# Kernel tuning notes

Measured on AMD Instinct MI355X. Metric: run time of the kernel, lower is better.

## Reference

```python
import jax, jax.numpy as jnp
import numpy as np

B, L, C, H = 2, 2048, 1024, 16
D = C // H
THETA = 50000.0


def rotate_half(x):
    x1, x2 = jnp.split(x, 2, axis=-1)
    return jnp.concatenate((-x2, x1), axis=-1)


def rope_freqs(n, dim):
    inv_freq = 1.0 / (THETA ** (jnp.arange(0, dim, 2, dtype=jnp.float32) / dim))
    freqs = jnp.arange(n, dtype=jnp.float32)[:, None] * inv_freq[None, :]  # [n, dim//2]
    return jnp.concatenate((freqs, freqs), axis=-1)  # [n, dim]


def setup_inputs() -> dict:
    key = jax.random.key(0)
    ks = jax.random.split(key, 8)
    q = jax.random.normal(ks[0], (B, L, C), dtype=jnp.float32)
    mask = jax.random.randint(ks[1], (B, L), 0, 2) > 0
    mask = mask.at[:, 0].set(True)  # avoid fully-masked rows
    s = 1.0 / np.sqrt(C)
    Wq = jax.random.normal(ks[2], (C, C), dtype=jnp.float32) * s
    Wk = jax.random.normal(ks[3], (C, C), dtype=jnp.float32) * s
    Wv = jax.random.normal(ks[4], (C, C), dtype=jnp.float32) * s
    Wo = jax.random.normal(ks[5], (C, C), dtype=jnp.float32) * s
    bo = jnp.zeros((C,), dtype=jnp.float32)
    return {"q": q, "mask": mask, "Wq": Wq, "Wk": Wk, "Wv": Wv, "Wo": Wo, "bo": bo}


def reference(q, mask, Wq, Wk, Wv, Wo, bo):
    x = q
    # QKV projections (torch Linear: y = x @ W.T)
    def proj(W):
        y = jnp.einsum('blc,oc->blo', x, W)
        return y.reshape(B, L, H, D).transpose(0, 2, 1, 3)  # [B,H,L,D]
    qh, kh, vh = proj(Wq), proj(Wk), proj(Wv)
    # RoPE (L == S)
    pos = rope_freqs(L, D)  # [L, D]
    cos, sin = jnp.cos(pos), jnp.sin(pos)
    qh = qh * cos + rotate_half(qh) * sin
    kh = kh * cos + rotate_half(kh) * sin
    # masked SDPA with additive bias (-inf where mask is False)
    scale = 1.0 / np.sqrt(D)
    bias = jnp.where(mask[:, None, None, :], 0.0, -jnp.inf)  # [B,1,1,S]
    scores = jnp.einsum('bhld,bhsd->bhls', qh, kh) * scale + bias
    attn = jax.nn.softmax(scores, axis=-1)
    out = jnp.einsum('bhls,bhsd->bhld', attn, vh)
    out = out.transpose(0, 2, 1, 3).reshape(B, L, C)
    return jnp.einsum('blc,oc->blo', out, Wo) + bo
```

## Files before the change

### kernel.cpp

```cpp
#include <hip/hip_runtime.h>
#include <hip/hip_bf16.h>

typedef __hip_bfloat16 bf16;
typedef short bf16x8 __attribute__((ext_vector_type(8)));
typedef short bf16x4 __attribute__((ext_vector_type(4)));
typedef float floatx4 __attribute__((ext_vector_type(4)));

#define Bb 2
#define Ll 2048
#define Cc 1024
#define Hh 16
#define Dd 64
#define INVFREQ_LN 0.3381180763f
#define QSCALE 0.125f

#define GLD16(gp, lp) __builtin_amdgcn_global_load_lds( \
    (const __attribute__((address_space(1))) void*)(gp), \
    (__attribute__((address_space(3))) void*)(lp), 16, 0, 0)

__device__ inline short f2bf(float f) {
    __hip_bfloat16 h = __float2bfloat16(f);
    return *reinterpret_cast<short*>(&h);
}
__device__ inline short f2bf_rn(float f) {
    return (short)((__float_as_uint(f) + 0x8000u) >> 16);
}

__global__ __launch_bounds__(256) void convert_bf16(
    const float* __restrict__ x, const float* __restrict__ wq,
    const float* __restrict__ wk, const float* __restrict__ wv,
    const float* __restrict__ wo,
    bf16* __restrict__ xb, bf16* __restrict__ wqkv, bf16* __restrict__ wob)
{
    const int XN = (Bb * Ll * Cc) / 8;
    const int WN = (Cc * Cc) / 8;
    int i = blockIdx.x * 256 + threadIdx.x;
    const float* src; bf16* dst;
    if (i < XN)               { src = x  + (size_t)i * 8;                 dst = xb   + (size_t)i * 8; }
    else if (i < XN + WN)     { int j = i - XN;        src = wq + (size_t)j * 8; dst = wqkv + (size_t)j * 8; }
    else if (i < XN + 2*WN)   { int j = i - XN - WN;   src = wk + (size_t)j * 8; dst = wqkv + (size_t)Cc*Cc     + (size_t)j * 8; }
    else if (i < XN + 3*WN)   { int j = i - XN - 2*WN; src = wv + (size_t)j * 8; dst = wqkv + (size_t)Cc*Cc*2   + (size_t)j * 8; }
    else                      { int j = i - XN - 3*WN; src = wo + (size_t)j * 8; dst = wob  + (size_t)j * 8; }
    float4 a = *reinterpret_cast<const float4*>(src);
    float4 b = *reinterpret_cast<const float4*>(src + 4);
    float vv[8] = {a.x, a.y, a.z, a.w, b.x, b.y, b.z, b.w};
    bf16x8 o;
    #pragma unroll
    for (int t = 0; t < 8; t++) o[t] = f2bf(vv[t]);
    *reinterpret_cast<bf16x8*>(dst) = o;
}

template <int MODE>
__global__ __launch_bounds__(256) void gemm_mfma(
    const bf16* __restrict__ A, const bf16* __restrict__ W,
    bf16* __restrict__ qb, bf16* __restrict__ kb, bf16* __restrict__ vb,
    float* __restrict__ outf, const float* __restrict__ bias,
    int M, int N, int K)
{
    __shared__ __align__(16) short As[128 * 32];
    __shared__ __align__(16) short Bs[128 * 32];

    const int tid  = threadIdx.x;
    const int wave = tid >> 6;
    const int lane = tid & 63;
    const int l15  = lane & 15;
    const int quad = lane >> 4;
    const int wm   = wave >> 1;
    const int wn   = wave & 1;
    const int m0   = blockIdx.y * 128;
    const int n0   = blockIdx.x * 128;

    const int ar = tid >> 2;
    const int ac = (tid & 3) * 8;

    floatx4 acc[4][4];
    #pragma unroll
    for (int mt = 0; mt < 4; mt++)
        #pragma unroll
        for (int nt = 0; nt < 4; nt++)
            #pragma unroll
            for (int r = 0; r < 4; r++) acc[mt][nt][r] = 0.f;

    for (int k0 = 0; k0 < K; k0 += 32) {
        __syncthreads();
        #pragma unroll
        for (int p = 0; p < 2; p++) {
            const bf16* gp = A + (size_t)(m0 + p * 64 + ar) * K + k0 + ac;
            GLD16(gp, &As[(p * 64 + ar) * 32 + ac]);
        }
        #pragma unroll
        for (int p = 0; p < 2; p++) {
            const bf16* gp = W + (size_t)(n0 + p * 64 + ar) * K + k0 + ac;
            GLD16(gp, &Bs[(p * 64 + ar) * 32 + ac]);
        }
        __syncthreads();

        bf16x8 af[4], bfr[4];
        #pragma unroll
        for (int mt = 0; mt < 4; mt++)
            af[mt] = *(const bf16x8*)&As[(wm * 64 + mt * 16 + l15) * 32 + quad * 8];
        #pragma unroll
        for (int nt = 0; nt < 4; nt++)
            bfr[nt] = *(const bf16x8*)&Bs[(wn * 64 + nt * 16 + l15) * 32 + quad * 8];
        #pragma unroll
        for (int mt = 0; mt < 4; mt++)
            #pragma unroll
            for (int nt = 0; nt < 4; nt++)
                acc[mt][nt] = __builtin_amdgcn_mfma_f32_16x16x32_bf16(
                    af[mt], bfr[nt], acc[mt][nt], 0, 0, 0);
    }

    if (MODE == 1) {
        #pragma unroll
        for (int mt = 0; mt < 4; mt++)
            #pragma unroll
            for (int r = 0; r < 4; r++) {
                int row = m0 + wm * 64 + mt * 16 + quad * 4 + r;
                #pragma unroll
                for (int nt = 0; nt < 4; nt++) {
                    int col = n0 + wn * 64 + nt * 16 + l15;
                    outf[(size_t)row * N + col] = acc[mt][nt][r] + bias[col];
                }
            }
    } else {
        const int colbase = n0 + wn * 64;
        const int which   = colbase >> 10;
        const int hh      = (colbase & (Cc - 1)) >> 6;
        if (which == 2) {
            #pragma unroll
            for (int mt = 0; mt < 4; mt++)
                #pragma unroll
                for (int r = 0; r < 4; r++) {
                    int row = m0 + wm * 64 + mt * 16 + quad * 4 + r;
                    int b = row >> 11, l = row & (Ll - 1);
                    size_t base = (size_t)(b * Hh + hh) * Dd * Ll + l;
                    #pragma unroll
                    for (int nt = 0; nt < 4; nt++) {
                        int d = nt * 16 + l15;
                        vb[base + (size_t)d * Ll] = __float2bfloat16(acc[mt][nt][r]);
                    }
                }
        } else {
            bf16* dst = which ? kb : qb;
            const float qs = which ? 1.0f : QSCALE;
            const float base0 = __expf(-(float)l15 * INVFREQ_LN);
            const float base1 = __expf(-(float)(l15 + 16) * INVFREQ_LN);
            #pragma unroll
            for (int mt = 0; mt < 4; mt++)
                #pragma unroll
                for (int r = 0; r < 4; r++) {
                    int row = m0 + wm * 64 + mt * 16 + quad * 4 + r;
                    int b = row >> 11, l = row & (Ll - 1);
                    size_t rb = ((size_t)(b * Hh + hh) * Ll + l) * Dd;
                    #pragma unroll
                    for (int nt2 = 0; nt2 < 2; nt2++) {
                        float fr = (float)l * (nt2 ? base1 : base0);
                        float sn, cs;
                        __sincosf(fr, &sn, &cs);
                        float x1 = acc[mt][nt2][r];
                        float x2 = acc[mt][nt2 + 2][r];
                        dst[rb + nt2 * 16 + l15]      = __float2bfloat16((x1 * cs - x2 * sn) * qs);
                        dst[rb + nt2 * 16 + l15 + 32] = __float2bfloat16((x2 * cs + x1 * sn) * qs);
                    }
                }
        }
    }
}

#define LSTR 72

__global__ __launch_bounds__(512) void attn_mfma(
    const bf16* __restrict__ q, const bf16* __restrict__ k, const bf16* __restrict__ vt,
    const int* __restrict__ mask, bf16* __restrict__ ctx)
{
    __shared__ __align__(16) short Ks[64 * LSTR];
    __shared__ __align__(16) short Vs[64 * LSTR];
    __shared__ __align__(16) short Ps[8][16 * LSTR];
    __shared__ __align__(16) float msk[64];

    const int tid  = threadIdx.x;
    const int wave = tid >> 6;
    const int lane = tid & 63;
    const int l15  = lane & 15;
    const int quad = lane >> 4;

    const int bh = blockIdx.x & 31;
    const int q0 = (blockIdx.x >> 5) << 7;
    const int b  = bh >> 4;
    const int h  = bh & (Hh - 1);

    const short* qb  = (const short*)(q  + (size_t)bh * Ll * Dd);
    const short* kb  = (const short*)(k  + (size_t)bh * Ll * Dd);
    const short* vtb = (const short*)(vt + (size_t)bh * Dd * Ll);
    const int* mrow = mask + b * Ll;

    const int qrow = q0 + wave * 16 + l15;
    bf16x8 qa0 = *(const bf16x8*)(qb + (size_t)qrow * Dd + quad * 8);
    bf16x8 qa1 = *(const bf16x8*)(qb + (size_t)qrow * Dd + 32 + quad * 8);

    floatx4 O[4];
    float l_r = 0.f;
    #pragma unroll
    for (int nt = 0; nt < 4; nt++)
        #pragma unroll
        for (int r = 0; r < 4; r++) O[nt][r] = 0.f;

    for (int s0 = 0; s0 < Ll; s0 += 64) {
        __syncthreads();
        {
            const int n  = tid >> 3;
            const int c8 = (tid & 7) << 3;
            *(bf16x8*)&Ks[n * LSTR + c8] =
                *(const bf16x8*)(kb + (size_t)(s0 + n) * Dd + c8);
        }
        {
            const int d = tid >> 3;
            const int o = (tid & 7) << 3;
            *(bf16x8*)&Vs[d * LSTR + o] =
                *(const bf16x8*)(vtb + (size_t)d * Ll + s0 + o);
        }
        if (tid < 64) msk[tid] = mrow[s0 + tid] ? 0.0f : -1e30f;
        __syncthreads();

        floatx4 S[4];
        #pragma unroll
        for (int nt = 0; nt < 4; nt++) {
            const short* krow = &Ks[(nt * 16 + l15) * LSTR + quad * 8];
            bf16x8 ka0 = *(const bf16x8*)krow;
            bf16x8 ka1 = *(const bf16x8*)(krow + 32);
            floatx4 acc; acc[0] = acc[1] = acc[2] = acc[3] = 0.f;
            acc = __builtin_amdgcn_mfma_f32_16x16x32_bf16(ka0, qa0, acc, 0, 0, 0);
            acc = __builtin_amdgcn_mfma_f32_16x16x32_bf16(ka1, qa1, acc, 0, 0, 0);
            S[nt] = acc;
        }

        #pragma unroll
        for (int nt = 0; nt < 4; nt++) {
            float4 m4 = *(const float4*)&msk[nt * 16 + quad * 4];
            float mv[4] = {m4.x, m4.y, m4.z, m4.w};
            bf16x4 pw;
            #pragma unroll
            for (int r = 0; r < 4; r++) {
                float p = __expf(S[nt][r] + mv[r]);
                l_r += p;
                pw[r] = f2bf_rn(p);
            }
            *(bf16x4*)&Ps[wave][l15 * LSTR + nt * 16 + quad * 4] = pw;
        }

        bf16x8 pb0 = *(const bf16x8*)&Ps[wave][l15 * LSTR + quad * 8];
        bf16x8 pb1 = *(const bf16x8*)&Ps[wave][l15 * LSTR + 32 + quad * 8];
        #pragma unroll
        for (int nt = 0; nt < 4; nt++) {
            const short* vrow = &Vs[(nt * 16 + l15) * LSTR + quad * 8];
            bf16x8 va0 = *(const bf16x8*)vrow;
            bf16x8 va1 = *(const bf16x8*)(vrow + 32);
            O[nt] = __builtin_amdgcn_mfma_f32_16x16x32_bf16(va0, pb0, O[nt], 0, 0, 0);
            O[nt] = __builtin_amdgcn_mfma_f32_16x16x32_bf16(va1, pb1, O[nt], 0, 0, 0);
        }
    }

    float l = l_r;
    l += __shfl_xor(l, 16);
    l += __shfl_xor(l, 32);
    const float inv = 1.0f / l;

    {
        int row = q0 + wave * 16 + l15;
        short* cp = (short*)ctx + ((size_t)(b * Ll + row)) * Cc + h * Dd;
        #pragma unroll
        for (int nt = 0; nt < 4; nt++) {
            bf16x4 ov;
            #pragma unroll
            for (int r = 0; r < 4; r++) ov[r] = f2bf_rn(O[nt][r] * inv);
            *(bf16x4*)&cp[nt * 16 + quad * 4] = ov;
        }
    }
}

extern "C" void kernel_launch(void* const* d_in, const int* in_sizes, int n_in,
                              void* d_out, int out_size, void* d_ws, size_t ws_size,
                              hipStream_t stream) {
    const float* x    = (const float*)d_in[0];
    const int*   mask = (const int*)d_in[1];
    const float* Wq   = (const float*)d_in[2];
    const float* Wk   = (const float*)d_in[3];
    const float* Wv   = (const float*)d_in[4];
    const float* Wo   = (const float*)d_in[5];
    const float* bo   = (const float*)d_in[6];
    float* out = (float*)d_out;

    const size_t per = (size_t)Bb * Hh * Ll * Dd;
    bf16* qbuf = (bf16*)d_ws;
    bf16* kbuf = qbuf + per;
    bf16* vbuf = kbuf + per;
    bf16* xb   = vbuf + per;
    bf16* wqkv = xb + per;
    bf16* wob  = wqkv + (size_t)3 * Cc * Cc;
    bf16* ctx  = xb;

    const int M = Bb * Ll;

    convert_bf16<<<(Bb*Ll*Cc/8 + 4*Cc*Cc/8) / 256, 256, 0, stream>>>(
        x, Wq, Wk, Wv, Wo, xb, wqkv, wob);

    dim3 gQKV(3 * Cc / 128, M / 128);
    gemm_mfma<0><<<gQKV, 256, 0, stream>>>(xb, wqkv, qbuf, kbuf, vbuf,
                                           nullptr, nullptr, M, 3 * Cc, Cc);

    attn_mfma<<<Bb * Hh * (Ll / 128), 512, 0, stream>>>(qbuf, kbuf, vbuf, mask, ctx);

    dim3 gOut(Cc / 128, M / 128);
    gemm_mfma<1><<<gOut, 256, 0, stream>>>(ctx, wob, nullptr, nullptr, nullptr,
                                           out, bo, M, Cc, Cc);
}
```

Baseline: 212.0 us.

## Double-buffer K/V tiles via direct global-to-LDS loads with XOR-swizzled layout

Result: faster. 202.9 us (-4.3%).

```diff
diff --git a/kernel.cpp b/kernel.cpp
--- a/kernel.cpp
+++ b/kernel.cpp
@@ -133,11 +133,14 @@
                 for (int r = 0; r < 4; r++) {
                     int row = m0 + wm * 64 + mt * 16 + quad * 4 + r;
                     int b = row >> 11, l = row & (Ll - 1);
-                    size_t base = (size_t)(b * Hh + hh) * Dd * Ll + l;
+                    size_t head = (size_t)(b * Hh + hh) * Dd * Ll;
+                    int lbase = (l & ~63) | (l & 7);
+                    int lg    = (l >> 3) & 7;
                     #pragma unroll
                     for (int nt = 0; nt < 4; nt++) {
                         int d = nt * 16 + l15;
-                        vb[base + (size_t)d * Ll] = __float2bfloat16(acc[mt][nt][r]);
+                        int pos = lbase | ((lg ^ (d & 7)) << 3);
+                        vb[head + (size_t)d * Ll + pos] = __float2bfloat16(acc[mt][nt][r]);
                     }
                 }
         } else {
@@ -159,8 +162,20 @@
                         __sincosf(fr, &sn, &cs);
                         float x1 = acc[mt][nt2][r];
                         float x2 = acc[mt][nt2 + 2][r];
-                        dst[rb + nt2 * 16 + l15]      = __float2bfloat16((x1 * cs - x2 * sn) * qs);
-                        dst[rb + nt2 * 16 + l15 + 32] = __float2bfloat16((x2 * cs + x1 * sn) * qs);
+                        float o1 = (x1 * cs - x2 * sn) * qs;
+                        float o2 = (x2 * cs + x1 * sn) * qs;
+                        int d1 = nt2 * 16 + l15;
+                        int d2 = d1 + 32;
+                        if (which == 1) {
+                            int sw = l & 7;
+                            int a1 = ((((d1 >> 3) ^ sw)) << 3) | (d1 & 7);
+                            int a2 = ((((d2 >> 3) ^ sw)) << 3) | (d2 & 7);
+                            dst[rb + a1] = __float2bfloat16(o1);
+                            dst[rb + a2] = __float2bfloat16(o2);
+                        } else {
+                            dst[rb + d1] = __float2bfloat16(o1);
+                            dst[rb + d2] = __float2bfloat16(o2);
+                        }
                     }
                 }
         }
@@ -173,10 +188,10 @@
     const bf16* __restrict__ q, const bf16* __restrict__ k, const bf16* __restrict__ vt,
     const int* __restrict__ mask, bf16* __restrict__ ctx)
 {
-    __shared__ __align__(16) short Ks[64 * LSTR];
-    __shared__ __align__(16) short Vs[64 * LSTR];
+    __shared__ __align__(16) short Ks[2][64 * 64];
+    __shared__ __align__(16) short Vs[2][64 * 64];
     __shared__ __align__(16) short Ps[8][16 * LSTR];
-    __shared__ __align__(16) float msk[64];
+    __shared__ __align__(16) float msk[2][64];
 
     const int tid  = threadIdx.x;
     const int wave = tid >> 6;
@@ -198,6 +213,14 @@
     bf16x8 qa0 = *(const bf16x8*)(qb + (size_t)qrow * Dd + quad * 8);
     bf16x8 qa1 = *(const bf16x8*)(qb + (size_t)qrow * Dd + 32 + quad * 8);
 
+    const int g0 = ((quad ^ (l15 & 7)) << 3);
+    const int g1 = (((quad + 4) ^ (l15 & 7)) << 3);
+
+    const short* vgp = vtb + (size_t)(tid >> 3) * Ll + ((tid & 7) << 3);
+    short* ksl = &Ks[0][0] + tid * 8;
+    short* vsl = &Vs[0][0] + tid * 8;
+    const int lbuf = 64 * 64;
+
     floatx4 O[4];
     float l_r = 0.f;
     #pragma unroll
@@ -205,29 +228,28 @@
         #pragma unroll
         for (int r = 0; r < 4; r++) O[nt][r] = 0.f;
 
-    for (int s0 = 0; s0 < Ll; s0 += 64) {
+    GLD16(kb + tid * 8, ksl);
+    GLD16(vgp, vsl);
+    if (tid < 64) msk[0][tid] = mrow[tid] ? 0.0f : -1e30f;
+
+    for (int t = 0; t < Ll / 64; t++) {
+        const int cur = t & 1;
         __syncthreads();
-        {
-            const int n  = tid >> 3;
-            const int c8 = (tid & 7) << 3;
-            *(bf16x8*)&Ks[n * LSTR + c8] =
-                *(const bf16x8*)(kb + (size_t)(s0 + n) * Dd + c8);
-        }
-        {
-            const int d = tid >> 3;
-            const int o = (tid & 7) << 3;
-            *(bf16x8*)&Vs[d * LSTR + o] =
-                *(const bf16x8*)(vtb + (size_t)d * Ll + s0 + o);
-        }
-        if (tid < 64) msk[tid] = mrow[s0 + tid] ? 0.0f : -1e30f;
-        __syncthreads();
-
+        if (t < Ll / 64 - 1) {
+            const int s1 = (t + 1) << 6;
+            GLD16(kb + (size_t)s1 * Dd + tid * 8, ksl + (cur ^ 1) * lbuf);
+            GLD16(vgp + s1,                       vsl + (cur ^ 1) * lbuf);
+            if (tid < 64) msk[cur ^ 1][tid] = mrow[s1 + tid] ? 0.0f : -1e30f;
+        }
+
+        const short* Kc = &Ks[cur][0];
+        const short* Vc = &Vs[cur][0];
         floatx4 S[4];
         #pragma unroll
         for (int nt = 0; nt < 4; nt++) {
-            const short* krow = &Ks[(nt * 16 + l15) * LSTR + quad * 8];
-            bf16x8 ka0 = *(const bf16x8*)krow;
-            bf16x8 ka1 = *(const bf16x8*)(krow + 32);
+            const short* krow = Kc + (nt * 16 + l15) * 64;
+            bf16x8 ka0 = *(const bf16x8*)(krow + g0);
+            bf16x8 ka1 = *(const bf16x8*)(krow + g1);
             floatx4 acc; acc[0] = acc[1] = acc[2] = acc[3] = 0.f;
             acc = __builtin_amdgcn_mfma_f32_16x16x32_bf16(ka0, qa0, acc, 0, 0, 0);
             acc = __builtin_amdgcn_mfma_f32_16x16x32_bf16(ka1, qa1, acc, 0, 0, 0);
@@ -236,7 +258,7 @@
 
         #pragma unroll
         for (int nt = 0; nt < 4; nt++) {
-            float4 m4 = *(const float4*)&msk[nt * 16 + quad * 4];
+            float4 m4 = *(const float4*)&msk[cur][nt * 16 + quad * 4];
             float mv[4] = {m4.x, m4.y, m4.z, m4.w};
             bf16x4 pw;
             #pragma unroll
@@ -252,9 +274,9 @@
         bf16x8 pb1 = *(const bf16x8*)&Ps[wave][l15 * LSTR + 32 + quad * 8];
         #pragma unroll
         for (int nt = 0; nt < 4; nt++) {
-            const short* vrow = &Vs[(nt * 16 + l15) * LSTR + quad * 8];
-            bf16x8 va0 = *(const bf16x8*)vrow;
-            bf16x8 va1 = *(const bf16x8*)(vrow + 32);
+            const short* vrow = Vc + (nt * 16 + l15) * 64;
+            bf16x8 va0 = *(const bf16x8*)(vrow + g0);
+            bf16x8 va1 = *(const bf16x8*)(vrow + g1);
             O[nt] = __builtin_amdgcn_mfma_f32_16x16x32_bf16(va0, pb0, O[nt], 0, 0, 0);
             O[nt] = __builtin_amdgcn_mfma_f32_16x16x32_bf16(va1, pb1, O[nt], 0, 0, 0);
         }
```
